# Kernel tuning notes

Measured on AMD Instinct MI355X. Metric: run time of the kernel, lower is better.

Reference implementation:

```python
import jax, jax.numpy as jnp
import numpy as np
from jax import lax

P = 8  # patch_size

def _conv(x, w, b, pad):
    y = lax.conv_general_dilated(x, w, (1, 1), [(pad, pad), (pad, pad)],
                                 dimension_numbers=('NCHW', 'OIHW', 'NCHW'))
    return y + b[None, :, None, None]

def _unfold(t):
    # t: [B,1,H,W] -> [B, L, P*P], matching torch.nn.Unfold(kernel=P, stride=P)
    B, _, H, W = t.shape
    t = t.reshape(B, H // P, P, W // P, P)
    t = t.transpose(0, 1, 3, 2, 4)
    return t.reshape(B, (H // P) * (W // P), P * P)

def setup_inputs() -> dict:
    key = jax.random.key(0)
    ks = jax.random.split(key, 10)
    d = {}
    d['x'] = jax.random.normal(ks[0], (4, 3, 512, 512), dtype=jnp.float32)
    d['fea'] = jax.random.normal(ks[1], (4, 64, 512, 512), dtype=jnp.float32)
    # conv_img: Conv2d(3,64,7x7,pad3) then Conv2d(64,1,3x3,pad1)
    d['w_img1'] = jax.random.normal(ks[2], (64, 3, 7, 7), dtype=jnp.float32) * 0.05
    d['b_img1'] = jax.random.normal(ks[3], (64,), dtype=jnp.float32) * 0.05
    d['w_img2'] = jax.random.normal(ks[4], (1, 64, 3, 3), dtype=jnp.float32) * 0.05
    d['b_img2'] = jax.random.normal(ks[5], (1,), dtype=jnp.float32) * 0.05
    # conv_feamap: Conv2d(64,1,1x1)
    d['w_fea'] = jax.random.normal(ks[6], (1, 64, 1, 1), dtype=jnp.float32) * 0.05
    d['b_fea'] = jax.random.normal(ks[7], (1,), dtype=jnp.float32) * 0.05
    # resolution_trans: Linear(P*P, 2*P*P, bias=False), Linear(2*P*P, P*P, bias=False), ReLU
    d['w1'] = jax.random.normal(ks[8], (2 * P * P, P * P), dtype=jnp.float32) * 0.1
    d['w2'] = jax.random.normal(ks[9], (P * P, 2 * P * P), dtype=jnp.float32) * 0.1
    return d

def reference(x, fea, w_img1, b_img1, w_img2, b_img2, w_fea, b_fea, w1, w2):
    ATT_DEPTH_SCALE = 4.0  # 2**att_depth * 2**att_depth with att_depth=1
    ini_img = _conv(_conv(x, w_img1, b_img1, 3), w_img2, b_img2, 1)      # [B,1,H,W]
    feamap = _conv(fea, w_fea, b_fea, 0) / ATT_DEPTH_SCALE               # [B,1,H,W]
    trans = lambda u: jax.nn.relu((u @ w1.T) @ w2.T)                     # [B,L,P*P]
    u_img = trans(_unfold(ini_img))
    u_fea = trans(_unfold(feamap))
    att = jnp.einsum('blp,bmp->blm', u_img, u_fea) / (P * P)             # [B,L,L]
    return att[:, None]                                                  # [B,1,L,L]
```

## Files before the change

kernel.cpp:

```cpp
#include <hip/hip_runtime.h>

#define IMG  262144
#define NPAT 4096

#define OFF_C9   0
#define OFF_W    256
#define OFF_INI  4352
#define OFF_FMAP (OFF_INI + 4*IMG)
#define OFF_V    (OFF_FMAP + 4*IMG)

typedef short v8s __attribute__((ext_vector_type(8)));
typedef float v4f __attribute__((ext_vector_type(4)));

__device__ inline unsigned short f2bf(float x) {
  unsigned u = __float_as_uint(x);
  u = u + 0x7FFF + ((u >> 16) & 1);
  return (unsigned short)(u >> 16);
}
__device__ inline float bf2f(unsigned short h) {
  return __uint_as_float(((unsigned)h) << 16);
}

__global__ __launch_bounds__(256) void k_compose(
    const float* __restrict__ w1img, const float* __restrict__ b1img,
    const float* __restrict__ w2img, const float* __restrict__ b2img,
    const float* __restrict__ w1,    const float* __restrict__ w2,
    float* __restrict__ ws) {
  int bid = blockIdx.x, tid = threadIdx.x;
  if (bid < 16) {
    int j = bid * 4 + (tid >> 6), q = tid & 63;
    float acc = 0.f;
    for (int k = 0; k < 128; ++k) acc += w2[j * 128 + k] * w1[k * 64 + q];
    ws[OFF_W + q * 64 + j] = acc;
    return;
  }
  if (tid < 243) {
    int i = tid / 81, r = tid % 81, dy = r / 9, dx = r % 9;
    float acc = 0.f;
    for (int m = 0; m < 64; ++m)
      for (int ky = 0; ky < 3; ++ky) {
        int k1y = dy - ky; if (k1y < 0 || k1y > 6) continue;
        for (int kx = 0; kx < 3; ++kx) {
          int k1x = dx - kx; if (k1x < 0 || k1x > 6) continue;
          acc += w2img[m * 9 + ky * 3 + kx] * w1img[(m * 3 + i) * 49 + k1y * 7 + k1x];
        }
      }
    ws[OFF_C9 + tid] = acc;
  } else if (tid == 243) {
    float acc = b2img[0];
    for (int m = 0; m < 64; ++m) {
      float s = 0.f;
      for (int k = 0; k < 9; ++k) s += w2img[m * 9 + k];
      acc += b1img[m] * s;
    }
    ws[OFF_C9 + 243] = acc;
  }
}

__global__ __launch_bounds__(256) void k_conv9(const float* __restrict__ x,
                                               const float* __restrict__ ws,
                                               float* __restrict__ ini) {
  __shared__ float sIn[3][24][72];
  int bid = blockIdx.x, tid = threadIdx.x;
  int b = bid >> 8, t = bid & 255;
  int ty0 = (t >> 3) << 4, tx0 = (t & 7) << 6;
  for (int idx = tid; idx < 3 * 24 * 72; idx += 256) {
    int c = idx / 1728, r = (idx % 1728) / 72, cc = idx % 72;
    int gy = ty0 + r - 4, gx = tx0 + cc - 4;
    float v = 0.f;
    if ((unsigned)gy < 512u && (unsigned)gx < 512u)
      v = x[(b * 3 + c) * IMG + gy * 512 + gx];
    sIn[c][r][cc] = v;
  }
  __syncthreads();
  const float* Cw = ws + OFF_C9;
  int ty = tid >> 4, tx = (tid & 15) << 2;
  float bc = Cw[243];
  float a0 = bc, a1 = bc, a2 = bc, a3 = bc;
  #pragma unroll
  for (int i = 0; i < 3; ++i)
    #pragma unroll
    for (int dy = 0; dy < 9; ++dy) {
      const float* rowp = &sIn[i][ty + dy][tx];
      float4 r0 = *(const float4*)rowp;
      float4 r1 = *(const float4*)(rowp + 4);
      float4 r2 = *(const float4*)(rowp + 8);
      float tt[12] = {r0.x, r0.y, r0.z, r0.w, r1.x, r1.y, r1.z, r1.w,
                      r2.x, r2.y, r2.z, r2.w};
      #pragma unroll
      for (int dx = 0; dx < 9; ++dx) {
        float w = Cw[i * 81 + dy * 9 + dx];
        a0 += w * tt[dx];     a1 += w * tt[dx + 1];
        a2 += w * tt[dx + 2]; a3 += w * tt[dx + 3];
      }
    }
  float4 o = {a0, a1, a2, a3};
  *(float4*)&ini[b * IMG + (ty0 + ty) * 512 + tx0 + tx] = o;
}

__global__ __launch_bounds__(256) void k_ring(const float* __restrict__ x,
                                              const float* __restrict__ w1img,
                                              const float* __restrict__ b1img,
                                              const float* __restrict__ w2img,
                                              float* __restrict__ ini) {
  int wid = blockIdx.x * 4 + (threadIdx.x >> 6);
  int lane = threadIdx.x & 63;
  int b = wid / 2044;
  int r = wid % 2044;
  int py, px;
  if (r < 512)       { py = 0;            px = r;        }
  else if (r < 1024) { py = 511;          px = r - 512;  }
  else if (r < 1534) { py = r - 1024 + 1; px = 0;        }
  else               { py = r - 1534 + 1; px = 511;      }
  int m = lane;
  float corr = 0.f;
  for (int k2y = 0; k2y < 3; ++k2y) {
    int qy = py + k2y - 1;
    for (int k2x = 0; k2x < 3; ++k2x) {
      int qx = px + k2x - 1;
      if (!(qy < 0 || qy >= 512 || qx < 0 || qx >= 512)) continue;
      float y1v = b1img[m];
      for (int i = 0; i < 3; ++i)
        for (int k1y = 0; k1y < 7; ++k1y) {
          int xy = qy + k1y - 3;
          if (xy < 0 || xy >= 512) continue;
          for (int k1x = 0; k1x < 7; ++k1x) {
            int xx = qx + k1x - 3;
            if (xx < 0 || xx >= 512) continue;
            y1v += w1img[(m * 3 + i) * 49 + k1y * 7 + k1x] * x[(b * 3 + i) * IMG + xy * 512 + xx];
          }
        }
      corr += w2img[m * 9 + k2y * 3 + k2x] * y1v;
    }
  }
  for (int off = 32; off > 0; off >>= 1) corr += __shfl_down(corr, off, 64);
  if (lane == 0) ini[b * IMG + py * 512 + px] -= corr;
}

__global__ __launch_bounds__(256) void k_feamap(const float* __restrict__ fea,
                                                const float* __restrict__ wfea,
                                                const float* __restrict__ bfea,
                                                float* __restrict__ fmap) {
  int pix = blockIdx.x * 1024 + threadIdx.x * 4;
  int b = pix >> 18;
  int rem = pix & (IMG - 1);
  const float* src = fea + (size_t)(b * 64) * IMG + rem;
  float4 acc = {0.f, 0.f, 0.f, 0.f};
  for (int c = 0; c < 64; ++c) {
    float w = wfea[c];
    float4 v = *(const float4*)(src + (size_t)c * IMG);
    acc.x += w * v.x; acc.y += w * v.y; acc.z += w * v.z; acc.w += w * v.w;
  }
  float bb = bfea[0];
  acc.x = (acc.x + bb) * 0.25f;
  acc.y = (acc.y + bb) * 0.25f;
  acc.z = (acc.z + bb) * 0.25f;
  acc.w = (acc.w + bb) * 0.25f;
  *(float4*)(fmap + pix) = acc;
}

__global__ __launch_bounds__(256) void k_trans(float* __restrict__ ws) {
  __shared__ float Us[64][68];
  int bid = blockIdx.x, tid = threadIdx.x;
  int s = bid >> 8, b = (bid >> 6) & 3, py = bid & 63;
  const float* src = ws + (s ? OFF_FMAP : OFF_INI) + b * IMG + py * 8 * 512;
  unsigned short* Vh = (unsigned short*)(ws + OFF_V) + (s ? 2097152 : 0) + b * NPAT * 64;
  unsigned short* Vl = Vh + 1048576;
  #pragma unroll
  for (int i = 0; i < 4; ++i) {
    int idx = tid + 256 * i;
    int row = idx >> 7;
    int c4  = (idx & 127) * 4;
    float4 v = *(const float4*)(src + row * 512 + c4);
    int px = c4 >> 3, c = c4 & 7;
    *(float4*)&Us[px][row * 8 + c] = v;
  }
  int j = tid & 63, wid = tid >> 6;
  float wc[64];
  #pragma unroll
  for (int q = 0; q < 64; ++q) wc[q] = ws[OFF_W + q * 64 + j];
  __syncthreads();
  #pragma unroll
  for (int i = 0; i < 16; ++i) {
    int lp = wid * 16 + i;
    float acc = 0.f;
    #pragma unroll
    for (int q4 = 0; q4 < 16; ++q4) {
      float4 u = *(const float4*)&Us[lp][q4 * 4];
      acc += u.x * wc[4*q4] + u.y * wc[4*q4+1] + u.z * wc[4*q4+2] + u.w * wc[4*q4+3];
    }
    acc = fmaxf(acc, 0.f);
    unsigned short h = f2bf(acc);
    unsigned short lo = f2bf(acc - bf2f(h));
    int lg = py * 64 + lp;
    Vh[lg * 64 + j] = h;
    Vl[lg * 64 + j] = lo;
  }
}

__global__ __launch_bounds__(256) void k_att(const float* __restrict__ ws,
                                             float* __restrict__ out) {
  __shared__ unsigned short lds[4][128][64];
  int bid = blockIdx.x, tid = threadIdx.x;
  int b = bid >> 10, t = bid & 1023;
  int l0 = (t >> 5) << 7, m0 = (t & 31) << 7;
  const unsigned short* V = (const unsigned short*)(ws + OFF_V);
  const unsigned short* pA_h = V + (b * NPAT + l0) * 64;
  const unsigned short* pA_l = V + 1048576 + (b * NPAT + l0) * 64;
  const unsigned short* pB_h = V + 2097152 + (b * NPAT + m0) * 64;
  const unsigned short* pB_l = V + 3145728 + (b * NPAT + m0) * 64;
  #pragma unroll
  for (int i = 0; i < 4; ++i) {
    int idx = tid + 256 * i;
    int row = idx >> 3, sg = idx & 7;
    int p = (sg ^ (row & 7)) * 8;
    *(uint4*)&lds[0][row][p] = *(const uint4*)(pA_h + row * 64 + sg * 8);
    *(uint4*)&lds[1][row][p] = *(const uint4*)(pA_l + row * 64 + sg * 8);
    *(uint4*)&lds[2][row][p] = *(const uint4*)(pB_h + row * 64 + sg * 8);
    *(uint4*)&lds[3][row][p] = *(const uint4*)(pB_l + row * 64 + sg * 8);
  }
  __syncthreads();
  int lane = tid & 63, wid = tid >> 6;
  int wm = (wid & 1) << 6, wn = (wid >> 1) << 6;
  int mlo = lane & 15, quad = lane >> 4;
  v4f acc[4][4] = {};
  #pragma unroll
  for (int kh = 0; kh < 2; ++kh) {
    int sL = quad + 4 * kh;
    v8s ah[4], al[4], bh[4], bl[4];
    #pragma unroll
    for (int mi = 0; mi < 4; ++mi) {
      int r = wm + mi * 16 + mlo;
      int p = (sL ^ (r & 7)) * 8;
      ah[mi] = *(const v8s*)&lds[0][r][p];
      al[mi] = *(const v8s*)&lds[1][r][p];
    }
    #pragma unroll
    for (int ni = 0; ni < 4; ++ni) {
      int r = wn + ni * 16 + mlo;
      int p = (sL ^ (r & 7)) * 8;
      bh[ni] = *(const v8s*)&lds[2][r][p];
      bl[ni] = *(const v8s*)&lds[3][r][p];
    }
    #pragma unroll
    for (int mi = 0; mi < 4; ++mi)
      #pragma unroll
      for (int ni = 0; ni < 4; ++ni) {
        acc[mi][ni] = __builtin_amdgcn_mfma_f32_16x16x32_bf16(ah[mi], bh[ni], acc[mi][ni], 0, 0, 0);
        acc[mi][ni] = __builtin_amdgcn_mfma_f32_16x16x32_bf16(ah[mi], bl[ni], acc[mi][ni], 0, 0, 0);
        acc[mi][ni] = __builtin_amdgcn_mfma_f32_16x16x32_bf16(al[mi], bh[ni], acc[mi][ni], 0, 0, 0);
      }
  }
  float* o = out + (size_t)b * 16777216;
  #pragma unroll
  for (int mi = 0; mi < 4; ++mi)
    #pragma unroll
    for (int ni = 0; ni < 4; ++ni) {
      int col = m0 + wn + ni * 16 + mlo;
      #pragma unroll
      for (int rr = 0; rr < 4; ++rr) {
        int row = l0 + wm + mi * 16 + quad * 4 + rr;
        o[(size_t)row * 4096 + col] = acc[mi][ni][rr] * 0.015625f;
      }
    }
}

extern "C" void kernel_launch(void* const* d_in, const int* in_sizes, int n_in,
                              void* d_out, int out_size, void* d_ws, size_t ws_size,
                              hipStream_t stream) {
  const float* x      = (const float*)d_in[0];
  const float* fea    = (const float*)d_in[1];
  const float* w_img1 = (const float*)d_in[2];
  const float* b_img1 = (const float*)d_in[3];
  const float* w_img2 = (const float*)d_in[4];
  const float* b_img2 = (const float*)d_in[5];
  const float* w_fea  = (const float*)d_in[6];
  const float* b_fea  = (const float*)d_in[7];
  const float* w1     = (const float*)d_in[8];
  const float* w2     = (const float*)d_in[9];
  float* ws  = (float*)d_ws;
  float* out = (float*)d_out;

  k_compose<<<17,   256, 0, stream>>>(w_img1, b_img1, w_img2, b_img2, w1, w2, ws);
  k_conv9  <<<1024, 256, 0, stream>>>(x, ws, ws + OFF_INI);
  k_ring   <<<2044, 256, 0, stream>>>(x, w_img1, b_img1, w_img2, ws + OFF_INI);
  k_feamap <<<1024, 256, 0, stream>>>(fea, w_fea, b_fea, ws + OFF_FMAP);
  k_trans  <<<512,  256, 0, stream>>>(ws);
  k_att    <<<4096, 256, 0, stream>>>(ws, out);
}
```

Measured before the change: 695.9 us.

## Fuse feamap into prep kernel, precompose ring weights, swizzle att blocks, nontemporal stores

Merges the 1x1 feature-map conv into the weight-composition kernel, so one launch does both and the small weight work runs alongside the bandwidth-bound fea read, which now uses nontemporal loads. Precomputes composed 3x3∘7x7 ring weights (G), so the border-correction kernel runs one thread per pixel instead of one 64-lane wave, dropping the shuffle reduction. Remaps att block order across XCD-style groups and writes the large 256MB output with nontemporal stores to cut cache pollution. These changes add some risk around extra workspace layout shifts and the block-ordering assumption.

```diff
diff --git a/kernel.cpp b/kernel.cpp
--- a/kernel.cpp
+++ b/kernel.cpp
@@ -5,7 +5,8 @@
 
 #define OFF_C9   0
 #define OFF_W    256
-#define OFF_INI  4352
+#define OFF_G    4352
+#define OFF_INI  5696
 #define OFF_FMAP (OFF_INI + 4*IMG)
 #define OFF_V    (OFF_FMAP + 4*IMG)
 
@@ -21,39 +22,73 @@
   return __uint_as_float(((unsigned)h) << 16);
 }
 
-__global__ __launch_bounds__(256) void k_compose(
+__global__ __launch_bounds__(256) void k_prep(
+    const float* __restrict__ fea,   const float* __restrict__ wfea,
+    const float* __restrict__ bfea,
     const float* __restrict__ w1img, const float* __restrict__ b1img,
     const float* __restrict__ w2img, const float* __restrict__ b2img,
     const float* __restrict__ w1,    const float* __restrict__ w2,
     float* __restrict__ ws) {
   int bid = blockIdx.x, tid = threadIdx.x;
-  if (bid < 16) {
-    int j = bid * 4 + (tid >> 6), q = tid & 63;
+  if (bid < 1024) {
+    int pix = bid * 1024 + tid * 4;
+    int b = pix >> 18;
+    int rem = pix & (IMG - 1);
+    const float* src = fea + (size_t)(b * 64) * IMG + rem;
+    v4f acc = {0.f, 0.f, 0.f, 0.f};
+    #pragma unroll 8
+    for (int c = 0; c < 64; ++c) {
+      float w = wfea[c];
+      v4f v = __builtin_nontemporal_load((const v4f*)(src + (size_t)c * IMG));
+      acc += w * v;
+    }
+    float bb = bfea[0];
+    acc = (acc + bb) * 0.25f;
+    *(v4f*)(ws + OFF_FMAP + pix) = acc;
+    return;
+  }
+  if (bid < 1040) {
+    int j = (bid - 1024) * 4 + (tid >> 6), q = tid & 63;
     float acc = 0.f;
     for (int k = 0; k < 128; ++k) acc += w2[j * 128 + k] * w1[k * 64 + q];
     ws[OFF_W + q * 64 + j] = acc;
     return;
   }
-  if (tid < 243) {
-    int i = tid / 81, r = tid % 81, dy = r / 9, dx = r % 9;
+  if (bid == 1040) {
+    if (tid < 243) {
+      int i = tid / 81, r = tid % 81, dy = r / 9, dx = r % 9;
+      float acc = 0.f;
+      for (int m = 0; m < 64; ++m)
+        for (int ky = 0; ky < 3; ++ky) {
+          int k1y = dy - ky; if (k1y < 0 || k1y > 6) continue;
+          for (int kx = 0; kx < 3; ++kx) {
+            int k1x = dx - kx; if (k1x < 0 || k1x > 6) continue;
+            acc += w2img[m * 9 + ky * 3 + kx] * w1img[(m * 3 + i) * 49 + k1y * 7 + k1x];
+          }
+        }
+      ws[OFF_C9 + tid] = acc;
+    } else if (tid == 243) {
+      float acc = b2img[0];
+      for (int m = 0; m < 64; ++m) {
+        float s = 0.f;
+        for (int k = 0; k < 9; ++k) s += w2img[m * 9 + k];
+        acc += b1img[m] * s;
+      }
+      ws[OFF_C9 + 243] = acc;
+    }
+    return;
+  }
+  int gidx = (bid - 1041) * 256 + tid;
+  if (gidx < 1323) {
+    int k2 = gidx / 147, t = gidx % 147;
     float acc = 0.f;
-    for (int m = 0; m < 64; ++m)
-      for (int ky = 0; ky < 3; ++ky) {
-        int k1y = dy - ky; if (k1y < 0 || k1y > 6) continue;
-        for (int kx = 0; kx < 3; ++kx) {
-          int k1x = dx - kx; if (k1x < 0 || k1x > 6) continue;
-          acc += w2img[m * 9 + ky * 3 + kx] * w1img[(m * 3 + i) * 49 + k1y * 7 + k1x];
-        }
-      }
-    ws[OFF_C9 + tid] = acc;
-  } else if (tid == 243) {
-    float acc = b2img[0];
-    for (int m = 0; m < 64; ++m) {
-      float s = 0.f;
-      for (int k = 0; k < 9; ++k) s += w2img[m * 9 + k];
-      acc += b1img[m] * s;
-    }
-    ws[OFF_C9 + 243] = acc;
+    for (int m = 0; m < 64; ++m) acc += w2img[m * 9 + k2] * w1img[m * 147 + t];
+    ws[OFF_G + gidx] = acc;
+  } else if (gidx < 1332) {
+    int k2 = gidx - 1323;
+    float acc = 0.f;
+    for (int m = 0; m < 64; ++m) acc += w2img[m * 9 + k2] * b1img[m];
+    ws[OFF_G + gidx] = acc;
   }
 }
 
@@ -99,64 +134,44 @@
 }
 
 __global__ __launch_bounds__(256) void k_ring(const float* __restrict__ x,
-                                              const float* __restrict__ w1img,
-                                              const float* __restrict__ b1img,
-                                              const float* __restrict__ w2img,
+                                              const float* __restrict__ ws,
                                               float* __restrict__ ini) {
-  int wid = blockIdx.x * 4 + (threadIdx.x >> 6);
-  int lane = threadIdx.x & 63;
-  int b = wid / 2044;
-  int r = wid % 2044;
+  int gid = blockIdx.x * 256 + threadIdx.x;
+  if (gid >= 4 * 2044) return;
+  int b = gid / 2044;
+  int r = gid % 2044;
   int py, px;
   if (r < 512)       { py = 0;            px = r;        }
   else if (r < 1024) { py = 511;          px = r - 512;  }
   else if (r < 1534) { py = r - 1024 + 1; px = 0;        }
   else               { py = r - 1534 + 1; px = 511;      }
-  int m = lane;
+  const float* G  = ws + OFF_G;
+  const float* Gb = G + 1323;
+  const float* xb = x + (size_t)(b * 3) * IMG;
   float corr = 0.f;
   for (int k2y = 0; k2y < 3; ++k2y) {
     int qy = py + k2y - 1;
     for (int k2x = 0; k2x < 3; ++k2x) {
       int qx = px + k2x - 1;
-      if (!(qy < 0 || qy >= 512 || qx < 0 || qx >= 512)) continue;
-      float y1v = b1img[m];
+      if (!((unsigned)qy >= 512u || (unsigned)qx >= 512u)) continue;
+      int k2 = k2y * 3 + k2x;
+      float acc = Gb[k2];
       for (int i = 0; i < 3; ++i)
         for (int k1y = 0; k1y < 7; ++k1y) {
           int xy = qy + k1y - 3;
-          if (xy < 0 || xy >= 512) continue;
+          if ((unsigned)xy >= 512u) continue;
+          const float* xrow = xb + i * IMG + xy * 512;
+          const float* Grow = G + k2 * 147 + i * 49 + k1y * 7;
           for (int k1x = 0; k1x < 7; ++k1x) {
             int xx = qx + k1x - 3;
-            if (xx < 0 || xx >= 512) continue;
-            y1v += w1img[(m * 3 + i) * 49 + k1y * 7 + k1x] * x[(b * 3 + i) * IMG + xy * 512 + xx];
+            if ((unsigned)xx >= 512u) continue;
+            acc += Grow[k1x] * xrow[xx];
           }
         }
-      corr += w2img[m * 9 + k2y * 3 + k2x] * y1v;
-    }
-  }
-  for (int off = 32; off > 0; off >>= 1) corr += __shfl_down(corr, off, 64);
-  if (lane == 0) ini[b * IMG + py * 512 + px] -= corr;
-}
-
-__global__ __launch_bounds__(256) void k_feamap(const float* __restrict__ fea,
-                                                const float* __restrict__ wfea,
-                                                const float* __restrict__ bfea,
-                                                float* __restrict__ fmap) {
-  int pix = blockIdx.x * 1024 + threadIdx.x * 4;
-  int b = pix >> 18;
-  int rem = pix & (IMG - 1);
-  const float* src = fea + (size_t)(b * 64) * IMG + rem;
-  float4 acc = {0.f, 0.f, 0.f, 0.f};
-  for (int c = 0; c < 64; ++c) {
-    float w = wfea[c];
-    float4 v = *(const float4*)(src + (size_t)c * IMG);
-    acc.x += w * v.x; acc.y += w * v.y; acc.z += w * v.z; acc.w += w * v.w;
-  }
-  float bb = bfea[0];
-  acc.x = (acc.x + bb) * 0.25f;
-  acc.y = (acc.y + bb) * 0.25f;
-  acc.z = (acc.z + bb) * 0.25f;
-  acc.w = (acc.w + bb) * 0.25f;
-  *(float4*)(fmap + pix) = acc;
+      corr += acc;
+    }
+  }
+  ini[b * IMG + py * 512 + px] -= corr;
 }
 
 __global__ __launch_bounds__(256) void k_trans(float* __restrict__ ws) {
@@ -201,7 +216,9 @@
 __global__ __launch_bounds__(256) void k_att(const float* __restrict__ ws,
                                              float* __restrict__ out) {
   __shared__ unsigned short lds[4][128][64];
-  int bid = blockIdx.x, tid = threadIdx.x;
+  int bid0 = blockIdx.x;
+  int bid = (bid0 & 7) * 512 + (bid0 >> 3);
+  int tid = threadIdx.x;
   int b = bid >> 10, t = bid & 1023;
   int l0 = (t >> 5) << 7, m0 = (t & 31) << 7;
   const unsigned short* V = (const unsigned short*)(ws + OFF_V);
@@ -260,7 +277,8 @@
       #pragma unroll
       for (int rr = 0; rr < 4; ++rr) {
         int row = l0 + wm + mi * 16 + quad * 4 + rr;
-        o[(size_t)row * 4096 + col] = acc[mi][ni][rr] * 0.015625f;
+        __builtin_nontemporal_store(acc[mi][ni][rr] * 0.015625f,
+                                    o + (size_t)row * 4096 + col);
       }
     }
 }
@@ -281,10 +299,10 @@
   float* ws  = (float*)d_ws;
   float* out = (float*)d_out;
 
-  k_compose<<<17,   256, 0, stream>>>(w_img1, b_img1, w_img2, b_img2, w1, w2, ws);
-  k_conv9  <<<1024, 256, 0, stream>>>(x, ws, ws + OFF_INI);
-  k_ring   <<<2044, 256, 0, stream>>>(x, w_img1, b_img1, w_img2, ws + OFF_INI);
-  k_feamap <<<1024, 256, 0, stream>>>(fea, w_fea, b_fea, ws + OFF_FMAP);
-  k_trans  <<<512,  256, 0, stream>>>(ws);
-  k_att    <<<4096, 256, 0, stream>>>(ws, out);
-}
+  k_prep  <<<1047, 256, 0, stream>>>(fea, w_fea, b_fea, w_img1, b_img1,
+                                     w_img2, b_img2, w1, w2, ws);
+  k_conv9 <<<1024, 256, 0, stream>>>(x, ws, ws + OFF_INI);
+  k_ring  <<<32,   256, 0, stream>>>(x, ws, ws + OFF_INI);
+  k_trans <<<512,  256, 0, stream>>>(ws);
+  k_att   <<<4096, 256, 0, stream>>>(ws, out);
+}
```

After: 591.8 us. -15.0%, faster.
